# Optimization experiments

Hardware: AMD Instinct MI355X
Metric: run time of the kernel (lower is better)

Reference implementation:

```python
import jax, jax.numpy as jnp
import numpy as np
from jax import lax

# 8-neighbor zero-pad offsets as (left, right, top, bottom), matching nn.ZeroPad2d args
PADS = [(0, 2, 0, 2), (1, 1, 0, 2), (2, 0, 0, 2), (0, 2, 1, 1),
        (2, 0, 1, 1), (0, 2, 2, 0), (1, 1, 2, 0), (2, 0, 2, 0)]
BN_EPS = 1e-5


def conv2d(x, w, pad):
    return lax.conv_general_dilated(x, w, (1, 1), [(pad, pad), (pad, pad)],
                                    dimension_numbers=('NCHW', 'OIHW', 'NCHW'))


def batchnorm(x, gamma, beta, mean, var):
    inv = gamma * lax.rsqrt(var + BN_EPS)
    return x * inv[None, :, None, None] + (beta - mean * inv)[None, :, None, None]


def resize_bilinear(x, oh, ow):
    # F.interpolate(mode='bilinear', align_corners=False)
    n, c, h, w = x.shape
    ys = jnp.clip((jnp.arange(oh, dtype=x.dtype) + 0.5) * (h / oh) - 0.5, 0.0, None)
    xs = jnp.clip((jnp.arange(ow, dtype=x.dtype) + 0.5) * (w / ow) - 0.5, 0.0, None)
    y0 = jnp.floor(ys); x0 = jnp.floor(xs)
    wy = (ys - y0)[:, None]; wx = (xs - x0)[None, :]
    y0i = jnp.clip(y0.astype(jnp.int32), 0, h - 1)
    y1i = jnp.clip(y0i + 1, 0, h - 1)
    x0i = jnp.clip(x0.astype(jnp.int32), 0, w - 1)
    x1i = jnp.clip(x0i + 1, 0, w - 1)
    r0 = x[:, :, y0i, :]; r1 = x[:, :, y1i, :]
    top = r0[:, :, :, x0i] * (1 - wx) + r0[:, :, :, x1i] * wx
    bot = r1[:, :, :, x0i] * (1 - wx) + r1[:, :, :, x1i] * wx
    return top * (1 - wy) + bot * wy


def lrwarp_error(left, disp, right):
    # Warp right image toward left using horizontal disparity (bilinear,
    # zero padding outside), then per-channel absolute photometric error.
    n, c, h, w = right.shape
    xs = jnp.arange(w, dtype=disp.dtype)[None, None, None, :] - disp  # [n,1,h,w]
    x0 = jnp.floor(xs)
    frac = xs - x0
    x0i = x0.astype(jnp.int32)
    x1i = x0i + 1
    v0 = ((x0i >= 0) & (x0i < w)).astype(right.dtype)
    v1 = ((x1i >= 0) & (x1i < w)).astype(right.dtype)
    x0c = jnp.broadcast_to(jnp.clip(x0i, 0, w - 1), (n, c, h, w))
    x1c = jnp.broadcast_to(jnp.clip(x1i, 0, w - 1), (n, c, h, w))
    g0 = jnp.take_along_axis(right, x0c, axis=3) * v0
    g1 = jnp.take_along_axis(right, x1c, axis=3) * v1
    warped = g0 * (1 - frac) + g1 * frac
    return jnp.abs(left - warped)


def setup_inputs() -> dict:
    key = jax.random.key(0)
    ks = jax.random.split(key, 16)
    N, H, W = 8, 256, 256
    inp = {
        'normal_estimation': jax.random.normal(ks[0], (N, 3, H, W), jnp.float32),
        'left_image': jax.random.uniform(ks[1], (N, 3, 512, 512), jnp.float32),
        'right_image': jax.random.uniform(ks[2], (N, 3, 512, 512), jnp.float32),
        'coarse_disparity': jax.random.uniform(ks[3], (N, 1, H, W), jnp.float32),
        'w1': jax.random.normal(ks[4], (32, 12, 3, 3), jnp.float32) * 0.1,
        'g1': jnp.ones((32,), jnp.float32), 'b1': jnp.zeros((32,), jnp.float32),
        'm1': jax.random.normal(ks[5], (32,), jnp.float32) * 0.01,
        'v1': jax.random.uniform(ks[6], (32,), jnp.float32, 0.5, 1.5),
        'w2': jax.random.normal(ks[7], (64, 32, 3, 3), jnp.float32) * 0.1,
        'g2': jnp.ones((64,), jnp.float32), 'b2': jnp.zeros((64,), jnp.float32),
        'm2': jax.random.normal(ks[8], (64,), jnp.float32) * 0.01,
        'v2': jax.random.uniform(ks[9], (64,), jnp.float32, 0.5, 1.5),
        'w3': jax.random.normal(ks[10], (8, 64, 1, 1), jnp.float32) * 0.1,
    }
    return inp


def _forward(normal_estimation, left_image, right_image, coarse_disparity,
             w1, g1, b1, m1, v1, w2, g2, b2, m2, v2, w3):
    H, W = coarse_disparity.shape[-2], coarse_disparity.shape[-1]
    cur_l = resize_bilinear(left_image, H, W)
    cur_r = resize_bilinear(right_image, H, W)
    disp_err = lrwarp_error(cur_l, coarse_disparity, cur_r)
    feats = jnp.concatenate([normal_estimation, cur_l, cur_r, disp_err], axis=1)
    x = jax.nn.relu(batchnorm(conv2d(feats, w1, 1), g1, b1, m1, v1))
    x = jax.nn.relu(batchnorm(conv2d(x, w2, 1), g2, b2, m2, v2))
    aff = jax.nn.relu(conv2d(x, w3, 0))  # [N,8,H,W]
    gate_p = jnp.stack([jnp.pad(aff[:, k], ((0, 0), (t, b), (l, r)))
                        for k, (l, r, t, b) in enumerate(PADS)], axis=1)
    d = coarse_disparity[:, 0]
    disp_p = jnp.stack([jnp.pad(d, ((0, 0), (t, b), (l, r)))
                        for (l, r, t, b) in PADS], axis=1)
    gate = jax.nn.softmax(gate_p, axis=1)
    prop = jnp.sum(gate * disp_p, axis=1, keepdims=True)[:, :, 1:-1, 1:-1]
    return prop * 0.3 + coarse_disparity * 0.7


def reference(normal_estimation, left_image, right_image, coarse_disparity,
              w1, g1, b1, m1, v1, w2, g2, b2, m2, v2, w3):
    return _forward(normal_estimation, left_image, right_image, coarse_disparity,
                    w1, g1, b1, m1, v1, w2, g2, b2, m2, v2, w3)
```

## Files before the change

### kernel.cpp

```cpp
#include <hip/hip_runtime.h>
#include <math.h>

#define NB 8
#define HH 256
#define WW 256
#define HW (HH*WW)

#define OFF_AFFB  0UL
#define OFF_W1FB  8388608UL
#define OFF_B1FB  8400896UL
#define OFF_W2FB  8401024UL
#define OFF_B2FB  8437888UL
#define OFF_W3FB  8438144UL
#define OFF_FEATS 8440192UL

typedef short  short8 __attribute__((ext_vector_type(8)));
typedef ushort u16x8  __attribute__((ext_vector_type(8)));
typedef ushort u16x4  __attribute__((ext_vector_type(4)));
typedef float  f32x4  __attribute__((ext_vector_type(4)));

__device__ __forceinline__ ushort f2bf(float x) {
  uint u = __float_as_uint(x);
  return (ushort)((u + 0x7FFFu + ((u >> 16) & 1u)) >> 16);
}
__device__ __forceinline__ float bf2f(ushort h) {
  uint u = ((uint)h) << 16;
  return __uint_as_float(u);
}

__global__ __launch_bounds__(256) void feats_row(
    const float* __restrict__ normal, const float* __restrict__ left,
    const float* __restrict__ right, const float* __restrict__ disp,
    const float* __restrict__ w1, const float* __restrict__ g1,
    const float* __restrict__ b1, const float* __restrict__ m1,
    const float* __restrict__ v1,
    const float* __restrict__ w2, const float* __restrict__ g2,
    const float* __restrict__ b2, const float* __restrict__ m2,
    const float* __restrict__ v2, const float* __restrict__ w3,
    char* __restrict__ wsb) {
  if (blockIdx.x >= 2048) {
    int idx = (blockIdx.x - 2048) * 256 + threadIdx.x;
    ushort* w1f = (ushort*)(wsb + OFF_W1FB);
    float* b1f  = (float*)(wsb + OFF_B1FB);
    ushort* w2f = (ushort*)(wsb + OFF_W2FB);
    float* b2f  = (float*)(wsb + OFF_B2FB);
    ushort* w3f = (ushort*)(wsb + OFF_W3FB);
    if (idx < 6144) {
      int jj = idx & 7;
      int lane = (idx >> 3) & 63;
      int nt = (idx >> 9) & 1;
      int s = idx >> 10;
      int ky = s >> 1, t = s & 1;
      int q = lane >> 4, lx = lane & 15;
      int k = q * 8 + jj;
      int dcol = k >> 4, ch = k & 15;
      int kx = t * 2 + dcol;
      int out = nt * 16 + lx;
      float inv = g1[out] / sqrtf(v1[out] + 1e-5f);
      float val = (ch < 12 && kx < 3) ? w1[((out * 12 + ch) * 3 + ky) * 3 + kx] * inv : 0.f;
      w1f[idx] = f2bf(val);
    }
    int j = idx - 6144;
    if (j >= 0 && j < 18432) {
      int kk   = j >> 11;
      int nt   = (j >> 9) & 3;
      int lane = (j >> 3) & 63;
      int jj   = j & 7;
      int q  = lane >> 4, lx = lane & 15;
      int cin = q * 8 + jj;
      int out = nt * 16 + lx;
      float inv = g2[out] / sqrtf(v2[out] + 1e-5f);
      w2f[j] = f2bf(w2[(out * 32 + cin) * 9 + kk] * inv);
      if (kk == 0 && q == 0 && jj == 0) b2f[out] = b2[out] - m2[out] * inv;
    }
    int k2 = idx - 24576;
    if (k2 >= 0 && k2 < 32) {
      float inv = g1[k2] / sqrtf(v1[k2] + 1e-5f);
      b1f[k2] = b1[k2] - m1[k2] * inv;
    }
    int k3 = idx - 24608;
    if (k3 >= 0 && k3 < 1024) {
      int jj = k3 & 7;
      int lane = (k3 >> 3) & 63;
      int slice = k3 >> 9;
      int q = lane >> 4, lx = lane & 15;
      int ch = slice * 32 + q * 8 + jj;
      w3f[k3] = (lx < 8) ? f2bf(w3[lx * 64 + ch]) : (ushort)0;
    }
    return;
  }
  __shared__ float curR[3][256];
  int blk = blockIdx.x;
  int n = blk >> 8;
  int i = blk & 255;
  int j = threadIdx.x;
  int i2 = i << 1;
  ushort* feats = (ushort*)(wsb + OFF_FEATS);
  float cl[3], cr[3];
#pragma unroll
  for (int c = 0; c < 3; ++c) {
    const float* Lp = left + ((size_t)(n * 3 + c) * 512 + i2) * 512 + (j << 1);
    float2 a0 = *(const float2*)Lp;
    float2 a1 = *(const float2*)(Lp + 512);
    cl[c] = 0.25f * (a0.x + a0.y + a1.x + a1.y);
    const float* Rp = right + ((size_t)(n * 3 + c) * 512 + i2) * 512 + (j << 1);
    float2 b0 = *(const float2*)Rp;
    float2 b1v = *(const float2*)(Rp + 512);
    cr[c] = 0.25f * (b0.x + b0.y + b1v.x + b1v.y);
    curR[c][j] = cr[c];
  }
  float nm[3];
#pragma unroll
  for (int c = 0; c < 3; ++c)
    nm[c] = normal[(size_t)(n * 3 + c) * HW + i * WW + j];
  float d = disp[(size_t)n * HW + i * WW + j];
  __syncthreads();
  float xs = (float)j - d;
  float x0f = floorf(xs);
  float fr = xs - x0f;
  int ix0 = (int)x0f;
  int ix1 = ix0 + 1;
  float vm0 = (ix0 >= 0 && ix0 < WW) ? 1.f : 0.f;
  float vm1 = (ix1 >= 0 && ix1 < WW) ? 1.f : 0.f;
  int x0c = min(max(ix0, 0), WW - 1);
  int x1c = min(max(ix1, 0), WW - 1);
  ushort tmp[16];
#pragma unroll
  for (int c = 0; c < 3; ++c) {
    float warped = curR[c][x0c] * vm0 * (1.f - fr) + curR[c][x1c] * vm1 * fr;
    tmp[9 + c] = f2bf(fabsf(cl[c] - warped));
    tmp[c] = f2bf(nm[c]);
    tmp[3 + c] = f2bf(cl[c]);
    tmp[6 + c] = f2bf(cr[c]);
  }
#pragma unroll
  for (int c = 12; c < 16; ++c) tmp[c] = 0;
  size_t ob = ((size_t)((n << 16) + i * WW + j)) * 16;
  *(u16x8*)&feats[ob] = *(u16x8*)&tmp[0];
  *(u16x8*)&feats[ob + 8] = *(u16x8*)&tmp[8];
}

__global__ __launch_bounds__(256) void trunk_kernel(char* __restrict__ wsb) {
  __shared__ ushort buf[18304];
  ushort* x1t = buf + 6464;
  const short8* __restrict__ w1fv = (const short8*)(wsb + OFF_W1FB);
  const float* __restrict__ b1f = (const float*)(wsb + OFF_B1FB);
  const short8* __restrict__ w2fv = (const short8*)(wsb + OFF_W2FB);
  const float* __restrict__ b2f = (const float*)(wsb + OFF_B2FB);
  const short8* __restrict__ w3fv = (const short8*)(wsb + OFF_W3FB);
  const ushort* __restrict__ feats = (const ushort*)(wsb + OFF_FEATS);
  ushort* aff = (ushort*)(wsb + OFF_AFFB);

  int blk = blockIdx.x;
  int n = blk >> 8;
  int t = blk & 255;
  int ty0 = (t >> 4) << 4;
  int tx0 = (t & 15) << 4;
  int tid = threadIdx.x;
  int lane = tid & 63;
  int wid = tid >> 6;
  int q = lane >> 4;
  int lx = lane & 15;

  if (tid < 8) *(u16x8*)&buf[(800 + tid) * 8] = (u16x8)0;
  for (int e = tid; e < 800; e += 256) {
    int row = e / 40;
    int rem = e - row * 40;
    int col = rem >> 1;
    int cc = rem & 1;
    int gy = ty0 + row - 2, gx = tx0 + col - 2;
    u16x8 v = (u16x8)0;
    if (gy >= 0 && gy < HH && gx >= 0 && gx < WW)
      v = *(const u16x8*)&feats[((size_t)((n << 16) + gy * WW + gx)) * 16 + cc * 8];
    int slot = e ^ ((e >> 3) & 7);
    *(u16x8*)&buf[slot * 8] = v;
  }
  __syncthreads();

  {
    short8 bw1[6][2];
#pragma unroll
    for (int s = 0; s < 6; ++s)
#pragma unroll
      for (int nt = 0; nt < 2; ++nt) bw1[s][nt] = w1fv[(s * 2 + nt) * 64 + lane];
    float bias1[2] = {b1f[lx], b1f[16 + lx]};
    for (int m = wid; m < 21; m += 4) {
      int pidx = min(m * 16 + lx, 323);
      int oyr = pidx / 18, oxr = pidx - oyr * 18;
      f32x4 a1[2];
      a1[0] = (f32x4)0.f; a1[1] = (f32x4)0.f;
#pragma unroll
      for (int s = 0; s < 6; ++s) {
        int ky = s >> 1, tt = s & 1;
        int G = ((oyr + ky) * 20 + oxr + tt * 2 + (q >> 1)) * 2 + (q & 1);
        int slot = G ^ ((G >> 3) & 7);
        short8 a = *(const short8*)&buf[slot * 8];
        a1[0] = __builtin_amdgcn_mfma_f32_16x16x32_bf16(a, bw1[s][0], a1[0], 0, 0, 0);
        a1[1] = __builtin_amdgcn_mfma_f32_16x16x32_bf16(a, bw1[s][1], a1[1], 0, 0, 0);
      }
#pragma unroll
      for (int r = 0; r < 4; ++r) {
        int p2 = m * 16 + q * 4 + r;
        if (p2 < 324) {
          int ry = p2 / 18, rx = p2 - ry * 18;
          int gy = ty0 + ry - 1, gx = tx0 + rx - 1;
          bool okp = (gy >= 0 && gy < HH && gx >= 0 && gx < WW);
#pragma unroll
          for (int nt = 0; nt < 2; ++nt) {
            float v = okp ? fmaxf(a1[nt][r] + bias1[nt], 0.f) : 0.f;
            x1t[(ry * 18 + rx) * 36 + nt * 16 + lx] = f2bf(v);
          }
        }
      }
    }
  }
  __syncthreads();

  f32x4 acc[4][4];
#pragma unroll
  for (int mt = 0; mt < 4; ++mt)
#pragma unroll
    for (int nt = 0; nt < 4; ++nt) acc[mt][nt] = (f32x4)0.f;
#pragma unroll
  for (int kk = 0; kk < 9; ++kk) {
    int ky = kk / 3, kx = kk - ky * 3;
    short8 a[4], b[4];
#pragma unroll
    for (int mt = 0; mt < 4; ++mt) {
      int row = wid * 4 + mt;
      a[mt] = *(const short8*)&x1t[((row + ky) * 18 + lx + kx) * 36 + q * 8];
    }
#pragma unroll
    for (int nt = 0; nt < 4; ++nt) b[nt] = w2fv[(kk * 4 + nt) * 64 + lane];
#pragma unroll
    for (int mt = 0; mt < 4; ++mt)
#pragma unroll
      for (int nt = 0; nt < 4; ++nt)
        acc[mt][nt] = __builtin_amdgcn_mfma_f32_16x16x32_bf16(a[mt], b[nt], acc[mt][nt], 0, 0, 0);
  }
  __syncthreads();

#pragma unroll
  for (int nt = 0; nt < 4; ++nt) {
    float bias = b2f[nt * 16 + lx];
#pragma unroll
    for (int mt = 0; mt < 4; ++mt) {
      int row = wid * 4 + mt;
#pragma unroll
      for (int r = 0; r < 4; ++r) {
        int p = row * 16 + q * 4 + r;
        float v = fmaxf(acc[mt][nt][r] + bias, 0.f);
        buf[p * 68 + nt * 16 + lx] = f2bf(v);
      }
    }
  }
  __syncthreads();

  short8 bw3[2];
  bw3[0] = w3fv[lane];
  bw3[1] = w3fv[64 + lane];
  f32x4 acc3[4];
#pragma unroll
  for (int mt = 0; mt < 4; ++mt) acc3[mt] = (f32x4)0.f;
#pragma unroll
  for (int mt = 0; mt < 4; ++mt) {
    int p = wid * 64 + mt * 16 + lx;
#pragma unroll
    for (int s = 0; s < 2; ++s) {
      short8 a3 = *(const short8*)&buf[p * 68 + s * 32 + q * 8];
      acc3[mt] = __builtin_amdgcn_mfma_f32_16x16x32_bf16(a3, bw3[s], acc3[mt], 0, 0, 0);
    }
  }
  if (lx < 8) {
#pragma unroll
    for (int mt = 0; mt < 4; ++mt) {
      int py = ty0 + wid * 4 + mt;
      int px = tx0 + q * 4;
      u16x4 pk;
#pragma unroll
      for (int r = 0; r < 4; ++r) pk[r] = f2bf(fmaxf(acc3[mt][r], 0.f));
      *(u16x4*)&aff[((size_t)(n * 8 + lx)) * HW + (size_t)py * WW + px] = pk;
    }
  }
}

__global__ __launch_bounds__(256) void final_kernel(const float* __restrict__ disp,
                                                    const char* __restrict__ wsb,
                                                    float* __restrict__ out) {
  int gid = blockIdx.x * 256 + threadIdx.x;
  int n = gid >> 14;
  int r = gid & 16383;
  int i = r >> 6;
  int j0 = (r & 63) << 2;
  const ushort* aff = (const ushort*)(wsb + OFF_AFFB);
  float d6[3][6];
#pragma unroll
  for (int rr = 0; rr < 3; ++rr) {
    int y = min(max(i + rr - 1, 0), HH - 1);
    const float* dp = disp + (size_t)n * HW + y * WW;
    float4 c4 = *(const float4*)(dp + j0);
    d6[rr][1] = c4.x; d6[rr][2] = c4.y; d6[rr][3] = c4.z; d6[rr][4] = c4.w;
    d6[rr][0] = dp[max(j0 - 1, 0)];
    d6[rr][5] = dp[min(j0 + 4, WW - 1)];
  }
  const int dy[8] = {1, 1, 1, 0, 0, -1, -1, -1};
  const int dx[8] = {1, 0, -1, 1, -1, 1, 0, -1};
  float g[8][4], dvv[8][4];
#pragma unroll
  for (int k = 0; k < 8; ++k) {
    int y = i + dy[k];
    bool vy = (y >= 0 && y < HH);
    int yc = min(max(y, 0), HH - 1);
    const ushort* ap = aff + ((size_t)(n * 8 + k)) * HW + (size_t)yc * WW;
    float w6[6];
    u16x4 c4 = *(const u16x4*)(ap + j0);
    w6[1] = bf2f(c4[0]); w6[2] = bf2f(c4[1]); w6[3] = bf2f(c4[2]); w6[4] = bf2f(c4[3]);
    w6[0] = bf2f(ap[max(j0 - 1, 0)]);
    w6[5] = bf2f(ap[min(j0 + 4, WW - 1)]);
    int rr = dy[k] + 1;
#pragma unroll
    for (int p = 0; p < 4; ++p) {
      int xp = j0 + p + dx[k];
      bool ok = vy && (xp >= 0) && (xp < WW);
      g[k][p] = ok ? w6[p + 1 + dx[k]] : 0.f;
      dvv[k][p] = ok ? d6[rr][p + 1 + dx[k]] : 0.f;
    }
  }
  float4 res;
#pragma unroll
  for (int p = 0; p < 4; ++p) {
    float m = g[0][p];
#pragma unroll
    for (int k = 1; k < 8; ++k) m = fmaxf(m, g[k][p]);
    float se = 0.f, sed = 0.f;
#pragma unroll
    for (int k = 0; k < 8; ++k) {
      float e = __expf(g[k][p] - m);
      se += e;
      sed += e * dvv[k][p];
    }
    float dc = d6[1][p + 1];
    (&res.x)[p] = 0.3f * (sed / se) + 0.7f * dc;
  }
  *(float4*)(out + (size_t)n * HW + i * WW + j0) = res;
}

extern "C" void kernel_launch(void* const* d_in, const int* in_sizes, int n_in,
                              void* d_out, int out_size, void* d_ws, size_t ws_size,
                              hipStream_t stream) {
  const float* normal = (const float*)d_in[0];
  const float* left   = (const float*)d_in[1];
  const float* right  = (const float*)d_in[2];
  const float* disp   = (const float*)d_in[3];
  const float* w1 = (const float*)d_in[4];
  const float* g1 = (const float*)d_in[5];
  const float* b1 = (const float*)d_in[6];
  const float* m1 = (const float*)d_in[7];
  const float* v1 = (const float*)d_in[8];
  const float* w2 = (const float*)d_in[9];
  const float* g2 = (const float*)d_in[10];
  const float* b2 = (const float*)d_in[11];
  const float* m2 = (const float*)d_in[12];
  const float* v2 = (const float*)d_in[13];
  const float* w3 = (const float*)d_in[14];
  char* wsb  = (char*)d_ws;
  float* out = (float*)d_out;

  hipLaunchKernelGGL(feats_row, dim3(2149), dim3(256), 0, stream,
                     normal, left, right, disp,
                     w1, g1, b1, m1, v1, w2, g2, b2, m2, v2, w3, wsb);
  hipLaunchKernelGGL(trunk_kernel, dim3(2048), dim3(256), 0, stream, wsb);
  hipLaunchKernelGGL(final_kernel, dim3(512), dim3(256), 0, stream, disp, wsb, out);
}
```

Before: 161.5 us.

## Process two pixels per thread in feats and pad conv2 LDS tile stride

The feature-building kernel now handles two rows per block and two adjacent pixels per thread. It uses float4 image loads, paired normal and disparity loads, and four 16-byte stores, which halves the block count. In the trunk kernel the intermediate activation tile's per-pixel stride in shared memory goes from 36 to 38 halves to reduce LDS bank conflicts, and the per-element index divisions are replaced by incremental row and column counters. The odd stride means the 16-byte shared-memory fragment reads are no longer 16-byte aligned, which may force the compiler to split them into smaller accesses.

```diff
diff --git a/kernel.cpp b/kernel.cpp
--- a/kernel.cpp
+++ b/kernel.cpp
@@ -38,8 +38,8 @@
     const float* __restrict__ b2, const float* __restrict__ m2,
     const float* __restrict__ v2, const float* __restrict__ w3,
     char* __restrict__ wsb) {
-  if (blockIdx.x >= 2048) {
-    int idx = (blockIdx.x - 2048) * 256 + threadIdx.x;
+  if (blockIdx.x >= 1024) {
+    int idx = (blockIdx.x - 1024) * 256 + threadIdx.x;
     ushort* w1f = (ushort*)(wsb + OFF_W1FB);
     float* b1f  = (float*)(wsb + OFF_B1FB);
     ushort* w2f = (ushort*)(wsb + OFF_W2FB);
@@ -89,59 +89,71 @@
     }
     return;
   }
-  __shared__ float curR[3][256];
+  __shared__ float curR[2][3][256];
   int blk = blockIdx.x;
-  int n = blk >> 8;
-  int i = blk & 255;
-  int j = threadIdx.x;
+  int n = blk >> 7;
+  int ir = (blk & 127) << 1;
+  int rs = threadIdx.x >> 7;
+  int t = threadIdx.x & 127;
+  int j0 = t << 1;
+  int i = ir + rs;
   int i2 = i << 1;
   ushort* feats = (ushort*)(wsb + OFF_FEATS);
-  float cl[3], cr[3];
+  ushort tmp[32];
+  float cl[2][3], cr[2][3];
 #pragma unroll
   for (int c = 0; c < 3; ++c) {
-    const float* Lp = left + ((size_t)(n * 3 + c) * 512 + i2) * 512 + (j << 1);
-    float2 a0 = *(const float2*)Lp;
-    float2 a1 = *(const float2*)(Lp + 512);
-    cl[c] = 0.25f * (a0.x + a0.y + a1.x + a1.y);
-    const float* Rp = right + ((size_t)(n * 3 + c) * 512 + i2) * 512 + (j << 1);
-    float2 b0 = *(const float2*)Rp;
-    float2 b1v = *(const float2*)(Rp + 512);
-    cr[c] = 0.25f * (b0.x + b0.y + b1v.x + b1v.y);
-    curR[c][j] = cr[c];
-  }
-  float nm[3];
-#pragma unroll
-  for (int c = 0; c < 3; ++c)
-    nm[c] = normal[(size_t)(n * 3 + c) * HW + i * WW + j];
-  float d = disp[(size_t)n * HW + i * WW + j];
-  __syncthreads();
-  float xs = (float)j - d;
-  float x0f = floorf(xs);
-  float fr = xs - x0f;
-  int ix0 = (int)x0f;
-  int ix1 = ix0 + 1;
-  float vm0 = (ix0 >= 0 && ix0 < WW) ? 1.f : 0.f;
-  float vm1 = (ix1 >= 0 && ix1 < WW) ? 1.f : 0.f;
-  int x0c = min(max(ix0, 0), WW - 1);
-  int x1c = min(max(ix1, 0), WW - 1);
-  ushort tmp[16];
-#pragma unroll
-  for (int c = 0; c < 3; ++c) {
-    float warped = curR[c][x0c] * vm0 * (1.f - fr) + curR[c][x1c] * vm1 * fr;
-    tmp[9 + c] = f2bf(fabsf(cl[c] - warped));
-    tmp[c] = f2bf(nm[c]);
-    tmp[3 + c] = f2bf(cl[c]);
-    tmp[6 + c] = f2bf(cr[c]);
-  }
-#pragma unroll
-  for (int c = 12; c < 16; ++c) tmp[c] = 0;
-  size_t ob = ((size_t)((n << 16) + i * WW + j)) * 16;
-  *(u16x8*)&feats[ob] = *(u16x8*)&tmp[0];
-  *(u16x8*)&feats[ob + 8] = *(u16x8*)&tmp[8];
+    const float* Lp = left + ((size_t)(n * 3 + c) * 512 + i2) * 512 + (j0 << 1);
+    float4 a0 = *(const float4*)Lp;
+    float4 a1 = *(const float4*)(Lp + 512);
+    cl[0][c] = 0.25f * (a0.x + a0.y + a1.x + a1.y);
+    cl[1][c] = 0.25f * (a0.z + a0.w + a1.z + a1.w);
+    const float* Rp = right + ((size_t)(n * 3 + c) * 512 + i2) * 512 + (j0 << 1);
+    float4 b0 = *(const float4*)Rp;
+    float4 b1v = *(const float4*)(Rp + 512);
+    cr[0][c] = 0.25f * (b0.x + b0.y + b1v.x + b1v.y);
+    cr[1][c] = 0.25f * (b0.z + b0.w + b1v.z + b1v.w);
+    curR[rs][c][j0] = cr[0][c];
+    curR[rs][c][j0 + 1] = cr[1][c];
+    float2 nm = *(const float2*)(normal + (size_t)(n * 3 + c) * HW + i * WW + j0);
+    tmp[c] = f2bf(nm.x);
+    tmp[16 + c] = f2bf(nm.y);
+    tmp[3 + c] = f2bf(cl[0][c]);
+    tmp[19 + c] = f2bf(cl[1][c]);
+    tmp[6 + c] = f2bf(cr[0][c]);
+    tmp[22 + c] = f2bf(cr[1][c]);
+  }
+  float2 dp2 = *(const float2*)(disp + (size_t)n * HW + i * WW + j0);
+  __syncthreads();
+#pragma unroll
+  for (int p = 0; p < 2; ++p) {
+    int j = j0 + p;
+    float d = p ? dp2.y : dp2.x;
+    float xs = (float)j - d;
+    float x0f = floorf(xs);
+    float fr = xs - x0f;
+    int ix0 = (int)x0f;
+    int ix1 = ix0 + 1;
+    float vm0 = (ix0 >= 0 && ix0 < WW) ? 1.f : 0.f;
+    float vm1 = (ix1 >= 0 && ix1 < WW) ? 1.f : 0.f;
+    int x0c = min(max(ix0, 0), WW - 1);
+    int x1c = min(max(ix1, 0), WW - 1);
+#pragma unroll
+    for (int c = 0; c < 3; ++c) {
+      float warped = curR[rs][c][x0c] * vm0 * (1.f - fr) + curR[rs][c][x1c] * vm1 * fr;
+      tmp[p * 16 + 9 + c] = f2bf(fabsf(cl[p][c] - warped));
+    }
+  }
+#pragma unroll
+  for (int c = 12; c < 16; ++c) { tmp[c] = 0; tmp[16 + c] = 0; }
+  size_t ob = ((size_t)((n << 16) + i * WW + j0)) * 16;
+#pragma unroll
+  for (int vv = 0; vv < 4; ++vv)
+    *(u16x8*)&feats[ob + vv * 8] = *(u16x8*)&tmp[vv * 8];
 }
 
 __global__ __launch_bounds__(256) void trunk_kernel(char* __restrict__ wsb) {
-  __shared__ ushort buf[18304];
+  __shared__ ushort buf[18784];
   ushort* x1t = buf + 6464;
   const short8* __restrict__ w1fv = (const short8*)(wsb + OFF_W1FB);
   const float* __restrict__ b1f = (const float*)(wsb + OFF_B1FB);
@@ -186,31 +198,36 @@
     float bias1[2] = {b1f[lx], b1f[16 + lx]};
     for (int m = wid; m < 21; m += 4) {
       int pidx = min(m * 16 + lx, 323);
-      int oyr = pidx / 18, oxr = pidx - oyr * 18;
+      int oyr = pidx / 18;
+      int Gbase = (pidx + 2 * oyr) * 2;
       f32x4 a1[2];
       a1[0] = (f32x4)0.f; a1[1] = (f32x4)0.f;
 #pragma unroll
       for (int s = 0; s < 6; ++s) {
         int ky = s >> 1, tt = s & 1;
-        int G = ((oyr + ky) * 20 + oxr + tt * 2 + (q >> 1)) * 2 + (q & 1);
+        int G = Gbase + (ky * 20 + tt * 2 + (q >> 1)) * 2 + (q & 1);
         int slot = G ^ ((G >> 3) & 7);
         short8 a = *(const short8*)&buf[slot * 8];
         a1[0] = __builtin_amdgcn_mfma_f32_16x16x32_bf16(a, bw1[s][0], a1[0], 0, 0, 0);
         a1[1] = __builtin_amdgcn_mfma_f32_16x16x32_bf16(a, bw1[s][1], a1[1], 0, 0, 0);
       }
+      int base = m * 16 + q * 4;
+      int ryb = base / 18;
+      int rxb = base - ryb * 18;
 #pragma unroll
       for (int r = 0; r < 4; ++r) {
-        int p2 = m * 16 + q * 4 + r;
+        int p2 = base + r;
         if (p2 < 324) {
-          int ry = p2 / 18, rx = p2 - ry * 18;
-          int gy = ty0 + ry - 1, gx = tx0 + rx - 1;
-          bool okp = (gy >= 0 && gy < HH && gx >= 0 && gx < WW);
+          int gy = ty0 + ryb - 1, gx = tx0 + rxb - 1;
+          bool okp = ((unsigned)gy < 256u) && ((unsigned)gx < 256u);
 #pragma unroll
           for (int nt = 0; nt < 2; ++nt) {
             float v = okp ? fmaxf(a1[nt][r] + bias1[nt], 0.f) : 0.f;
-            x1t[(ry * 18 + rx) * 36 + nt * 16 + lx] = f2bf(v);
+            x1t[p2 * 38 + nt * 16 + lx] = f2bf(v);
           }
         }
+        ++rxb;
+        if (rxb == 18) { rxb = 0; ++ryb; }
       }
     }
   }
@@ -228,7 +245,7 @@
 #pragma unroll
     for (int mt = 0; mt < 4; ++mt) {
       int row = wid * 4 + mt;
-      a[mt] = *(const short8*)&x1t[((row + ky) * 18 + lx + kx) * 36 + q * 8];
+      a[mt] = *(const short8*)&x1t[((row + ky) * 18 + lx + kx) * 38 + q * 8];
     }
 #pragma unroll
     for (int nt = 0; nt < 4; ++nt) b[nt] = w2fv[(kk * 4 + nt) * 64 + lane];
@@ -366,7 +383,7 @@
   char* wsb  = (char*)d_ws;
   float* out = (float*)d_out;
 
-  hipLaunchKernelGGL(feats_row, dim3(2149), dim3(256), 0, stream,
+  hipLaunchKernelGGL(feats_row, dim3(1125), dim3(256), 0, stream,
                      normal, left, right, disp,
                      w1, g1, b1, m1, v1, w2, g2, b2, m2, v2, w3, wsb);
   hipLaunchKernelGGL(trunk_kernel, dim3(2048), dim3(256), 0, stream, wsb);
```

Measured after the change: 173.5 us. 1.07x slower.
